# Performance work log

Measured on AMD Instinct MI355X. Metric: run time of the kernel, lower is better.

Reference implementation:

```python
import jax, jax.numpy as jnp
import numpy as np

IN_DIM, K, NB = 64, 32, 16
N = NB * K
BATCH = 32768
DT = 0.05
TAU_EPS = 1e-6


def _xavier(key, shape):
    fan_in, fan_out = shape[-1], shape[-2]
    lim = np.sqrt(6.0 / (fan_in + fan_out)).astype(np.float32)
    return jax.random.uniform(key, shape, jnp.float32, -lim, lim)


def setup_inputs() -> dict:
    key = jax.random.key(0)
    ks = jax.random.split(key, 8)
    return {
        "y": jax.random.normal(ks[0], (BATCH, N), jnp.float32),
        "u_t": jax.random.normal(ks[1], (BATCH, IN_DIM), jnp.float32),
        "W_in": _xavier(ks[2], (K, IN_DIM)),            # (out, in) like nn.Linear
        "b_in": jnp.zeros((K,), jnp.float32),
        "W_fwd": _xavier(ks[3], (NB - 1, K, K)),        # stacked per-block (out, in)
        "b_fwd": jnp.zeros((NB - 1, K), jnp.float32),
        "W_rec": _xavier(ks[4], (NB, K, K)),
        "b_rec": jnp.zeros((NB, K), jnp.float32),
        "E_l": _xavier(ks[5], (NB, K, K)),
        "E_l_r": _xavier(ks[6], (NB, K, K)),
        "tau_raw": jnp.zeros((N,), jnp.float32),
        "n_steps": 8,
    }


def reference(y, u_t, W_in, b_in, W_fwd, b_fwd, W_rec, b_rec, E_l, E_l_r, tau_raw, n_steps):
    batch = y.shape[0]
    nb, k = E_l.shape[0], E_l.shape[1]
    yb = y.reshape(batch, nb, k)
    # time constant (constant across Euler steps)
    inv_tau = 1.0 / (jax.nn.softplus(tau_raw) + TAU_EPS)
    inv_tau = inv_tau.reshape(nb, k)
    # block-0 input drive (depends only on u_t, so constant across steps)
    net0 = jnp.tanh(u_t @ W_in.T + b_in)  # [batch, k]

    def step(yb, _):
        prev = yb[:, :-1, :]  # blocks 0..nb-2 feed blocks 1..nb-1
        net_fwd = jnp.tanh(jnp.einsum("bjk,jlk->bjl", prev, W_fwd) + b_fwd)
        net_out = jnp.concatenate([net0[:, None, :], net_fwd], axis=1)  # [batch, nb, k]
        net_rec = jnp.tanh(jnp.einsum("bjk,jlk->bjl", yb, W_rec) + b_rec)
        decay = inv_tau + jnp.abs(net_out) + jnp.abs(net_rec)
        out_term = jnp.einsum("jlk,bjk->bjl", E_l, net_out)
        rec_term = jnp.einsum("jlk,bjk->bjl", E_l_r, net_rec)
        yb_new = yb + DT * (-yb * decay + out_term + rec_term)
        return yb_new, None

    yb, _ = jax.lax.scan(step, yb, None, length=n_steps)
    return yb.reshape(batch, nb * k)
```

## Files before the change

kernel.cpp:

```cpp
#include <hip/hip_runtime.h>
#include <hip/hip_bf16.h>
#include <math.h>

#define NBLK 16
#define KD 32
#define NDIM 512
#define INDIM 64
#define DT_C 0.05f
#define TAU_EPS_C 1e-6f
#define MROWS 16
#define WGSIZE 1024


typedef __attribute__((ext_vector_type(8))) short bf16x8;
typedef __attribute__((ext_vector_type(4))) float f32x4;
typedef __attribute__((ext_vector_type(4))) unsigned int u32x4;

#define MFMA16(a,b,c) __builtin_amdgcn_mfma_f32_16x16x32_bf16((a),(b),(c),0,0,0)

__device__ __forceinline__ float fast_tanh(float x){
    float e = __expf(2.0f * x);
    return 1.0f - 2.0f / (e + 1.0f);
}
__device__ __forceinline__ unsigned int pack_bf2_fast(float a, float b){
    unsigned int ua = __float_as_uint(a) + 0x8000u;
    unsigned int ub = __float_as_uint(b) + 0x8000u;
    return __builtin_amdgcn_perm(ua, ub, 0x03020706);
}
__device__ __forceinline__ unsigned short f2bf(float f){
    __hip_bfloat16 h = __float2bfloat16(f);
    return *reinterpret_cast<unsigned short*>(&h);
}

union FragU { bf16x8 h; u32x4 u; };

__device__ __forceinline__ bf16x8 pack8_fast(const float* a, const float* b){
    FragU z;
    z.u.x = pack_bf2_fast(a[0], a[1]);
    z.u.y = pack_bf2_fast(a[2], a[3]);
    z.u.z = pack_bf2_fast(b[0], b[1]);
    z.u.w = pack_bf2_fast(b[2], b[3]);
    return z.h;
}
__device__ __forceinline__ bf16x8 pack8_rne(f32x4 a, f32x4 b){
    bf16x8 r;
    r[0]=(short)f2bf(a[0]); r[1]=(short)f2bf(a[1]); r[2]=(short)f2bf(a[2]); r[3]=(short)f2bf(a[3]);
    r[4]=(short)f2bf(b[0]); r[5]=(short)f2bf(b[1]); r[6]=(short)f2bf(b[2]); r[7]=(short)f2bf(b[3]);
    return r;
}
__device__ __forceinline__ bf16x8 afrag_pi(const float* __restrict__ Wrow, int q){
    f32x4 lo = *(const f32x4*)(Wrow + q*4);
    f32x4 hi = *(const f32x4*)(Wrow + 16 + q*4);
    return pack8_rne(lo, hi);
}

__global__ __launch_bounds__(WGSIZE, 4)
void ltcn_kernel(const float* __restrict__ y_in,
                 const float* __restrict__ u_t,
                 const float* __restrict__ W_in,
                 const float* __restrict__ b_in,
                 const float* __restrict__ W_fwd,
                 const float* __restrict__ b_fwd,
                 const float* __restrict__ W_rec,
                 const float* __restrict__ b_rec,
                 const float* __restrict__ E_l,
                 const float* __restrict__ E_l_r,
                 const float* __restrict__ tau_raw,
                 const int* __restrict__ n_steps_p,
                 float* __restrict__ y_out,
                 int batch)
{
    __shared__ u32x4 Ylds[2 * NBLK * 64];

    const int tid  = threadIdx.x;
    const int j    = tid >> 6;
    const int lane = tid & 63;
    const int q    = lane >> 4;
    const int b15  = lane & 15;
    const int ns   = n_steps_p[0];

    const float* Wr = W_rec + (size_t)j * KD * KD;
    const float* Wf = W_fwd + (size_t)((j > 0) ? (j-1) : 0) * KD * KD;
    const float* Ee = E_l   + (size_t)j * KD * KD;
    const float* Er = E_l_r + (size_t)j * KD * KD;

    bf16x8 Arec[2], Afwd[2], AEl[2], AElr[2];
    f32x4  cR[2], cF[2];
    float  itau[2][4];
    #pragma unroll
    for (int f = 0; f < 2; ++f){
        const int row = f*16 + b15;
        Arec[f] = afrag_pi(Wr + row*KD, q);
        Afwd[f] = afrag_pi(Wf + row*KD, q);
        AEl[f]  = afrag_pi(Ee + row*KD, q);
        AElr[f] = afrag_pi(Er + row*KD, q);
        #pragma unroll
        for (int r = 0; r < 4; ++r){
            const int lp = f*16 + q*4 + r;
            cR[f][r] = b_rec[j*KD + lp];
            cF[f][r] = (j > 0) ? b_fwd[(j-1)*KD + lp] : 0.f;
            float tr = tau_raw[j*KD + lp];
            float sp = fmaxf(tr, 0.f) + log1pf(__expf(-fabsf(tr)));
            itau[f][r] = 1.0f / (sp + TAU_EPS_C);
        }
    }
    const f32x4 zero = {0.f, 0.f, 0.f, 0.f};
    const int tiles = batch / MROWS;

    for (int t = blockIdx.x; t < tiles; t += gridDim.x){
        const int row0 = t * MROWS;

        float yv[2][4];
        #pragma unroll
        for (int f = 0; f < 2; ++f){
            f32x4 tmp = *(const f32x4*)&y_in[(size_t)(row0 + b15)*NDIM + j*KD + f*16 + q*4];
            #pragma unroll
            for (int r = 0; r < 4; ++r) yv[f][r] = tmp[r];
        }

        bf16x8 AO0 = {0,0,0,0,0,0,0,0};
        float dec0[2][4];
        if (j == 0){
            f32x4 acc[2];
            #pragma unroll
            for (int f = 0; f < 2; ++f)
            #pragma unroll
            for (int r = 0; r < 4; ++r) acc[f][r] = b_in[f*16 + q*4 + r];
            #pragma unroll
            for (int c = 0; c < 2; ++c){
                const float* up = &u_t[(size_t)(row0 + b15)*INDIM + c*32 + q*8];
                bf16x8 uB = pack8_rne(*(const f32x4*)up, *(const f32x4*)(up + 4));
                #pragma unroll
                for (int f = 0; f < 2; ++f){
                    const float* wp = &W_in[(size_t)(f*16 + b15)*INDIM + c*32 + q*8];
                    bf16x8 wA = pack8_rne(*(const f32x4*)wp, *(const f32x4*)(wp + 4));
                    acc[f] = MFMA16(wA, uB, acc[f]);
                }
            }
            float n0[2][4];
            #pragma unroll
            for (int f = 0; f < 2; ++f)
            #pragma unroll
            for (int r = 0; r < 4; ++r){
                float v = fast_tanh(acc[f][r]);
                n0[f][r] = v;
                dec0[f][r] = itau[f][r] + fabsf(v);
            }
            AO0 = pack8_fast(n0[0], n0[1]);
        }

        int cur = 0;
        for (int s = 0; s < ns; ++s){
            bf16x8 yB = pack8_fast(yv[0], yv[1]);
            FragU yu; yu.h = yB;
            Ylds[cur*(NBLK*64) + j*64 + lane] = yu.u;
            __syncthreads();

            bf16x8 AO; float dec[2][4];
            if (j > 0){
                FragU pv; pv.u = Ylds[cur*(NBLK*64) + (j-1)*64 + lane];
                f32x4 a0 = MFMA16(Afwd[0], pv.h, cF[0]);
                f32x4 a1 = MFMA16(Afwd[1], pv.h, cF[1]);
                float nf[2][4];
                #pragma unroll
                for (int r = 0; r < 4; ++r){
                    nf[0][r] = fast_tanh(a0[r]);
                    nf[1][r] = fast_tanh(a1[r]);
                    dec[0][r] = itau[0][r] + fabsf(nf[0][r]);
                    dec[1][r] = itau[1][r] + fabsf(nf[1][r]);
                }
                AO = pack8_fast(nf[0], nf[1]);
            } else {
                AO = AO0;
                #pragma unroll
                for (int r = 0; r < 4; ++r){ dec[0][r] = dec0[0][r]; dec[1][r] = dec0[1][r]; }
            }

            f32x4 g0 = MFMA16(Arec[0], yB, cR[0]);
            f32x4 g1 = MFMA16(Arec[1], yB, cR[1]);
            float nr[2][4];
            #pragma unroll
            for (int r = 0; r < 4; ++r){
                nr[0][r] = fast_tanh(g0[r]);
                nr[1][r] = fast_tanh(g1[r]);
                dec[0][r] += fabsf(nr[0][r]);
                dec[1][r] += fabsf(nr[1][r]);
            }
            bf16x8 AR = pack8_fast(nr[0], nr[1]);

            f32x4 o0 = MFMA16(AEl[0], AO, MFMA16(AElr[0], AR, zero));
            f32x4 o1 = MFMA16(AEl[1], AO, MFMA16(AElr[1], AR, zero));
            #pragma unroll
            for (int r = 0; r < 4; ++r){
                yv[0][r] = fmaf(DT_C, fmaf(-yv[0][r], dec[0][r], o0[r]), yv[0][r]);
                yv[1][r] = fmaf(DT_C, fmaf(-yv[1][r], dec[1][r], o1[r]), yv[1][r]);
            }
            cur ^= 1;
        }

        #pragma unroll
        for (int f = 0; f < 2; ++f){
            f32x4 sv = {yv[f][0], yv[f][1], yv[f][2], yv[f][3]};
            *(f32x4*)&y_out[(size_t)(row0 + b15)*NDIM + j*KD + f*16 + q*4] = sv;
        }
    }
}

extern "C" void kernel_launch(void* const* d_in, const int* in_sizes, int n_in,
                              void* d_out, int out_size, void* d_ws, size_t ws_size,
                              hipStream_t stream) {
    const float* y       = (const float*)d_in[0];
    const float* u_t     = (const float*)d_in[1];
    const float* W_in    = (const float*)d_in[2];
    const float* b_in    = (const float*)d_in[3];
    const float* W_fwd   = (const float*)d_in[4];
    const float* b_fwd   = (const float*)d_in[5];
    const float* W_rec   = (const float*)d_in[6];
    const float* b_rec   = (const float*)d_in[7];
    const float* E_l     = (const float*)d_in[8];
    const float* E_l_r   = (const float*)d_in[9];
    const float* tau_raw = (const float*)d_in[10];
    const int*   n_steps = (const int*)d_in[11];
    float* out = (float*)d_out;

    const int batch = in_sizes[0] / NDIM;
    const int grid  = 256;

    hipLaunchKernelGGL(ltcn_kernel, dim3(grid), dim3(WGSIZE), 0, stream,
                       y, u_t, W_in, b_in, W_fwd, b_fwd, W_rec, b_rec,
                       E_l, E_l_r, tau_raw, n_steps, out, batch);
}
```

Before: 307.4 us.

## Process two row tiles per workgroup iteration and use hardware exp2/rcp tanh

```diff
diff --git a/kernel.cpp b/kernel.cpp
--- a/kernel.cpp
+++ b/kernel.cpp
@@ -19,8 +19,9 @@
 #define MFMA16(a,b,c) __builtin_amdgcn_mfma_f32_16x16x32_bf16((a),(b),(c),0,0,0)
 
 __device__ __forceinline__ float fast_tanh(float x){
-    float e = __expf(2.0f * x);
-    return 1.0f - 2.0f / (e + 1.0f);
+    float e = __builtin_amdgcn_exp2f(x * 2.885390081777927f);
+    float r = __builtin_amdgcn_rcpf(e + 1.0f);
+    return fmaf(-2.0f, r, 1.0f);
 }
 __device__ __forceinline__ unsigned int pack_bf2_fast(float a, float b){
     unsigned int ua = __float_as_uint(a) + 0x8000u;
@@ -70,7 +71,7 @@
                  float* __restrict__ y_out,
                  int batch)
 {
-    __shared__ u32x4 Ylds[2 * NBLK * 64];
+    __shared__ u32x4 Ylds[2][2][NBLK * 64];
 
     const int tid  = threadIdx.x;
     const int j    = tid >> 6;
@@ -105,103 +106,129 @@
         }
     }
     const f32x4 zero = {0.f, 0.f, 0.f, 0.f};
-    const int tiles = batch / MROWS;
-
-    for (int t = blockIdx.x; t < tiles; t += gridDim.x){
-        const int row0 = t * MROWS;
-
-        float yv[2][4];
+    const int pairs = (batch / MROWS) / 2;
+
+    int cur = 0;
+
+    for (int p = blockIdx.x; p < pairs; p += gridDim.x){
+        const int row0A = (2*p)     * MROWS;
+        const int row0B = (2*p + 1) * MROWS;
+
+        float yv[2][2][4];
         #pragma unroll
         for (int f = 0; f < 2; ++f){
-            f32x4 tmp = *(const f32x4*)&y_in[(size_t)(row0 + b15)*NDIM + j*KD + f*16 + q*4];
-            #pragma unroll
-            for (int r = 0; r < 4; ++r) yv[f][r] = tmp[r];
-        }
-
-        bf16x8 AO0 = {0,0,0,0,0,0,0,0};
-        float dec0[2][4];
+            f32x4 ta = *(const f32x4*)&y_in[(size_t)(row0A + b15)*NDIM + j*KD + f*16 + q*4];
+            f32x4 tb = *(const f32x4*)&y_in[(size_t)(row0B + b15)*NDIM + j*KD + f*16 + q*4];
+            #pragma unroll
+            for (int r = 0; r < 4; ++r){ yv[0][f][r] = ta[r]; yv[1][f][r] = tb[r]; }
+        }
+
+        bf16x8 AO0[2] = {{0,0,0,0,0,0,0,0},{0,0,0,0,0,0,0,0}};
         if (j == 0){
-            f32x4 acc[2];
-            #pragma unroll
-            for (int f = 0; f < 2; ++f)
-            #pragma unroll
-            for (int r = 0; r < 4; ++r) acc[f][r] = b_in[f*16 + q*4 + r];
-            #pragma unroll
-            for (int c = 0; c < 2; ++c){
-                const float* up = &u_t[(size_t)(row0 + b15)*INDIM + c*32 + q*8];
-                bf16x8 uB = pack8_rne(*(const f32x4*)up, *(const f32x4*)(up + 4));
-                #pragma unroll
-                for (int f = 0; f < 2; ++f){
-                    const float* wp = &W_in[(size_t)(f*16 + b15)*INDIM + c*32 + q*8];
-                    bf16x8 wA = pack8_rne(*(const f32x4*)wp, *(const f32x4*)(wp + 4));
-                    acc[f] = MFMA16(wA, uB, acc[f]);
-                }
-            }
-            float n0[2][4];
-            #pragma unroll
-            for (int f = 0; f < 2; ++f)
-            #pragma unroll
-            for (int r = 0; r < 4; ++r){
-                float v = fast_tanh(acc[f][r]);
-                n0[f][r] = v;
-                dec0[f][r] = itau[f][r] + fabsf(v);
-            }
-            AO0 = pack8_fast(n0[0], n0[1]);
-        }
-
-        int cur = 0;
+            #pragma unroll
+            for (int u = 0; u < 2; ++u){
+                const int r0 = u ? row0B : row0A;
+                f32x4 acc[2];
+                #pragma unroll
+                for (int f = 0; f < 2; ++f)
+                #pragma unroll
+                for (int r = 0; r < 4; ++r) acc[f][r] = b_in[f*16 + q*4 + r];
+                #pragma unroll
+                for (int c = 0; c < 2; ++c){
+                    const float* up = &u_t[(size_t)(r0 + b15)*INDIM + c*32 + q*8];
+                    bf16x8 uB = pack8_rne(*(const f32x4*)up, *(const f32x4*)(up + 4));
+                    #pragma unroll
+                    for (int f = 0; f < 2; ++f){
+                        const float* wp = &W_in[(size_t)(f*16 + b15)*INDIM + c*32 + q*8];
+                        bf16x8 wA = pack8_rne(*(const f32x4*)wp, *(const f32x4*)(wp + 4));
+                        acc[f] = MFMA16(wA, uB, acc[f]);
+                    }
+                }
+                float n0[2][4];
+                #pragma unroll
+                for (int f = 0; f < 2; ++f)
+                #pragma unroll
+                for (int r = 0; r < 4; ++r) n0[f][r] = fast_tanh(acc[f][r]);
+                AO0[u] = pack8_fast(n0[0], n0[1]);
+            }
+        }
+
         for (int s = 0; s < ns; ++s){
-            bf16x8 yB = pack8_fast(yv[0], yv[1]);
-            FragU yu; yu.h = yB;
-            Ylds[cur*(NBLK*64) + j*64 + lane] = yu.u;
+            bf16x8 yB[2];
+            #pragma unroll
+            for (int u = 0; u < 2; ++u){
+                yB[u] = pack8_fast(yv[u][0], yv[u][1]);
+                FragU w; w.h = yB[u];
+                Ylds[cur][u][j*64 + lane] = w.u;
+            }
             __syncthreads();
 
-            bf16x8 AO; float dec[2][4];
+            float dec[2][2][4];
+            bf16x8 AO[2];
             if (j > 0){
-                FragU pv; pv.u = Ylds[cur*(NBLK*64) + (j-1)*64 + lane];
-                f32x4 a0 = MFMA16(Afwd[0], pv.h, cF[0]);
-                f32x4 a1 = MFMA16(Afwd[1], pv.h, cF[1]);
-                float nf[2][4];
+                #pragma unroll
+                for (int u = 0; u < 2; ++u){
+                    FragU pv; pv.u = Ylds[cur][u][(j-1)*64 + lane];
+                    f32x4 a0 = MFMA16(Afwd[0], pv.h, cF[0]);
+                    f32x4 a1 = MFMA16(Afwd[1], pv.h, cF[1]);
+                    float nf[2][4];
+                    #pragma unroll
+                    for (int r = 0; r < 4; ++r){
+                        nf[0][r] = fast_tanh(a0[r]);
+                        nf[1][r] = fast_tanh(a1[r]);
+                        dec[u][0][r] = itau[0][r] + fabsf(nf[0][r]);
+                        dec[u][1][r] = itau[1][r] + fabsf(nf[1][r]);
+                    }
+                    AO[u] = pack8_fast(nf[0], nf[1]);
+                }
+            } else {
+                #pragma unroll
+                for (int u = 0; u < 2; ++u){
+                    AO[u] = AO0[u];
+                    FragU w; w.h = AO0[u];
+                    unsigned int ws[4] = {w.u.x, w.u.y, w.u.z, w.u.w};
+                    #pragma unroll
+                    for (int f = 0; f < 2; ++f)
+                    #pragma unroll
+                    for (int r = 0; r < 4; ++r){
+                        unsigned int word = ws[f*2 + (r >> 1)];
+                        unsigned int bits = (r & 1) ? (word & 0xFFFF0000u) : (word << 16);
+                        dec[u][f][r] = itau[f][r] + fabsf(__uint_as_float(bits));
+                    }
+                }
+            }
+
+            #pragma unroll
+            for (int u = 0; u < 2; ++u){
+                f32x4 g0 = MFMA16(Arec[0], yB[u], cR[0]);
+                f32x4 g1 = MFMA16(Arec[1], yB[u], cR[1]);
+                float nr[2][4];
                 #pragma unroll
                 for (int r = 0; r < 4; ++r){
-                    nf[0][r] = fast_tanh(a0[r]);
-                    nf[1][r] = fast_tanh(a1[r]);
-                    dec[0][r] = itau[0][r] + fabsf(nf[0][r]);
-                    dec[1][r] = itau[1][r] + fabsf(nf[1][r]);
-                }
-                AO = pack8_fast(nf[0], nf[1]);
-            } else {
-                AO = AO0;
-                #pragma unroll
-                for (int r = 0; r < 4; ++r){ dec[0][r] = dec0[0][r]; dec[1][r] = dec0[1][r]; }
-            }
-
-            f32x4 g0 = MFMA16(Arec[0], yB, cR[0]);
-            f32x4 g1 = MFMA16(Arec[1], yB, cR[1]);
-            float nr[2][4];
-            #pragma unroll
-            for (int r = 0; r < 4; ++r){
-                nr[0][r] = fast_tanh(g0[r]);
-                nr[1][r] = fast_tanh(g1[r]);
-                dec[0][r] += fabsf(nr[0][r]);
-                dec[1][r] += fabsf(nr[1][r]);
-            }
-            bf16x8 AR = pack8_fast(nr[0], nr[1]);
-
-            f32x4 o0 = MFMA16(AEl[0], AO, MFMA16(AElr[0], AR, zero));
-            f32x4 o1 = MFMA16(AEl[1], AO, MFMA16(AElr[1], AR, zero));
-            #pragma unroll
-            for (int r = 0; r < 4; ++r){
-                yv[0][r] = fmaf(DT_C, fmaf(-yv[0][r], dec[0][r], o0[r]), yv[0][r]);
-                yv[1][r] = fmaf(DT_C, fmaf(-yv[1][r], dec[1][r], o1[r]), yv[1][r]);
+                    nr[0][r] = fast_tanh(g0[r]);
+                    nr[1][r] = fast_tanh(g1[r]);
+                    dec[u][0][r] += fabsf(nr[0][r]);
+                    dec[u][1][r] += fabsf(nr[1][r]);
+                }
+                bf16x8 AR = pack8_fast(nr[0], nr[1]);
+
+                f32x4 o0 = MFMA16(AEl[0], AO[u], MFMA16(AElr[0], AR, zero));
+                f32x4 o1 = MFMA16(AEl[1], AO[u], MFMA16(AElr[1], AR, zero));
+                #pragma unroll
+                for (int r = 0; r < 4; ++r){
+                    yv[u][0][r] = fmaf(DT_C, fmaf(-yv[u][0][r], dec[u][0][r], o0[r]), yv[u][0][r]);
+                    yv[u][1][r] = fmaf(DT_C, fmaf(-yv[u][1][r], dec[u][1][r], o1[r]), yv[u][1][r]);
+                }
             }
             cur ^= 1;
         }
 
         #pragma unroll
         for (int f = 0; f < 2; ++f){
-            f32x4 sv = {yv[f][0], yv[f][1], yv[f][2], yv[f][3]};
-            *(f32x4*)&y_out[(size_t)(row0 + b15)*NDIM + j*KD + f*16 + q*4] = sv;
+            f32x4 sa = {yv[0][f][0], yv[0][f][1], yv[0][f][2], yv[0][f][3]};
+            f32x4 sb = {yv[1][f][0], yv[1][f][1], yv[1][f][2], yv[1][f][3]};
+            *(f32x4*)&y_out[(size_t)(row0A + b15)*NDIM + j*KD + f*16 + q*4] = sa;
+            *(f32x4*)&y_out[(size_t)(row0B + b15)*NDIM + j*KD + f*16 + q*4] = sb;
         }
     }
 }
```

After: 297.3 us. 1.03x faster.
